# Performance work log

Hardware: AMD Instinct MI355X
Metric: run time of the kernel (lower is better)

Reference implementation:

```python
import jax, jax.numpy as jnp
import numpy as np

N_NODES = 50000
N_EDGES = 800000
D_FEAT = 64
N_AGENTS = 1024
A_DIM = 16
MSG = 128          # msg_dim
OUT = 128          # out_dim


def _w(k, fan_in, fan_out):
    return jax.random.normal(k, (fan_in, fan_out), jnp.float32) / np.sqrt(fan_in).astype(np.float32)


def setup_inputs() -> dict:
    key = jax.random.key(0)
    ks = jax.random.split(key, 24)
    inp = {}
    inp["x"] = jax.random.normal(ks[0], (N_NODES, D_FEAT), jnp.float32)
    inp["actions"] = jax.random.normal(ks[1], (N_AGENTS, A_DIM), jnp.float32)
    inp["senders"] = jax.random.randint(ks[2], (N_EDGES,), 0, N_NODES, jnp.int32)
    inp["receivers"] = jax.random.randint(ks[3], (N_EDGES,), 0, N_NODES, jnp.int32)
    inp["n_agents"] = N_AGENTS
    # message MLP: concat(sender, receiver) -> 256 -> 256 -> msg_dim
    inp["W_m1"] = _w(ks[4], 2 * D_FEAT, 256); inp["b_m1"] = jnp.zeros((256,), jnp.float32)
    inp["W_m2"] = _w(ks[5], 256, 256);        inp["b_m2"] = jnp.zeros((256,), jnp.float32)
    inp["W_m3"] = _w(ks[6], 256, MSG);        inp["b_m3"] = jnp.zeros((MSG,), jnp.float32)
    # aggregation MLP: msg_dim -> 128 -> 128 -> msg_dim
    inp["W_a1"] = _w(ks[7], MSG, 128);        inp["b_a1"] = jnp.zeros((128,), jnp.float32)
    inp["W_a2"] = _w(ks[8], 128, 128);        inp["b_a2"] = jnp.zeros((128,), jnp.float32)
    inp["W_a3"] = _w(ks[9], 128, MSG);        inp["b_a3"] = jnp.zeros((MSG,), jnp.float32)
    # update MLP: concat(node, aggregated) -> 256 -> 256 -> out_dim
    inp["W_u1"] = _w(ks[10], D_FEAT + MSG, 256); inp["b_u1"] = jnp.zeros((256,), jnp.float32)
    inp["W_u2"] = _w(ks[11], 256, 256);          inp["b_u2"] = jnp.zeros((256,), jnp.float32)
    inp["W_u3"] = _w(ks[12], 256, OUT);          inp["b_u3"] = jnp.zeros((OUT,), jnp.float32)
    # critic head
    inp["W_act"] = _w(ks[13], A_DIM, 128);    inp["b_act"] = jnp.zeros((128,), jnp.float32)
    inp["W_h1"] = _w(ks[14], OUT + 128, 256); inp["b_h1"] = jnp.zeros((256,), jnp.float32)
    inp["W_h2"] = _w(ks[15], 256, 256);       inp["b_h2"] = jnp.zeros((256,), jnp.float32)
    inp["W_q"] = _w(ks[16], 256, 1);          inp["b_q"] = jnp.zeros((1,), jnp.float32)
    return inp


def reference(x, actions, senders, receivers, n_agents,
              W_m1, b_m1, W_m2, b_m2, W_m3, b_m3,
              W_a1, b_a1, W_a2, b_a2, W_a3, b_a3,
              W_u1, b_u1, W_u2, b_u2, W_u3, b_u3,
              W_act, b_act, W_h1, b_h1, W_h2, b_h2, W_q, b_q):
    relu = jax.nn.relu
    # --- GNN layer: edge messages (gather endpoints, MLP) ---
    h = jnp.concatenate([x[senders], x[receivers]], axis=-1)   # [E, 2*D]
    h = relu(h @ W_m1 + b_m1)
    h = relu(h @ W_m2 + b_m2)
    msg = h @ W_m3 + b_m3                                      # [E, MSG]
    # --- aggregate messages at receivers (scatter-add) ---
    aggr = jax.ops.segment_sum(msg, receivers, num_segments=x.shape[0])  # [N, MSG]
    a = relu(aggr @ W_a1 + b_a1)
    a = relu(a @ W_a2 + b_a2)
    a = a @ W_a3 + b_a3                                        # [N, MSG]
    # --- node update ---
    u = jnp.concatenate([x, a], axis=-1)                       # [N, D+MSG]
    u = relu(u @ W_u1 + b_u1)
    u = relu(u @ W_u2 + b_u2)
    feats = (u @ W_u3 + b_u3)[:n_agents]                       # agent (type-0) nodes
    # --- critic head ---
    ap = relu(actions @ W_act + b_act)                         # [n_agents, 128]
    z = jnp.concatenate([feats, ap], axis=-1)
    z = relu(z @ W_h1 + b_h1)
    z = relu(z @ W_h2 + b_h2)
    q = z @ W_q + b_q
    return jnp.squeeze(q, axis=-1)                             # [n_agents]
```

## Files before the change

### kernel.cpp

```cpp
#include <hip/hip_runtime.h>
#include <hip/hip_bf16.h>


#define STRIDE 260

typedef __attribute__((ext_vector_type(8))) short short8;
typedef __attribute__((ext_vector_type(4))) float floatx4;

union Frag8 { short8 s; uint u[4]; };

__device__ __forceinline__ void cvt_hi_lo(const float4 f0, const float4 f1,
                                          Frag8& hi, Frag8& lo) {
    uint U[8] = { __float_as_uint(f0.x), __float_as_uint(f0.y),
                  __float_as_uint(f0.z), __float_as_uint(f0.w),
                  __float_as_uint(f1.x), __float_as_uint(f1.y),
                  __float_as_uint(f1.z), __float_as_uint(f1.w) };
    float F[8] = { f0.x, f0.y, f0.z, f0.w, f1.x, f1.y, f1.z, f1.w };
#pragma unroll
    for (int p = 0; p < 4; ++p) {
        uint a = U[2*p], b = U[2*p+1];
        hi.u[p] = (a >> 16) | (b & 0xFFFF0000u);
        float l0 = F[2*p]   - __uint_as_float(a & 0xFFFF0000u);
        float l1 = F[2*p+1] - __uint_as_float(b & 0xFFFF0000u);
        __hip_bfloat162 pl = __float22bfloat162_rn(make_float2(l0, l1));
        union { __hip_bfloat162 h; uint v; } cvt; cvt.h = pl;
        lo.u[p] = cvt.v;
    }
}

__global__ void pack_weights(const float* __restrict__ Wm1,
                             const float* __restrict__ Wm2,
                             const float* __restrict__ Wm3,
                             uint* __restrict__ pack) {
    int g = blockIdx.x * 256 + threadIdx.x;
    const float* W; int NOUT, NT, local; uint *dhi, *dlo;
    if (g < 4096)       { W = Wm1; NOUT = 256; NT = 16; local = g;         dhi = pack;          dlo = pack + 16384; }
    else if (g < 12288) { W = Wm2; NOUT = 256; NT = 16; local = g - 4096;  dhi = pack + 32768;  dlo = pack + 65536; }
    else                { W = Wm3; NOUT = 128; NT = 8;  local = g - 12288; dhi = pack + 98304;  dlo = pack + 114688; }
    int lane = local & 63;
    int tmp  = local >> 6;
    int nt = tmp % NT, kb = tmp / NT;
    int n  = nt * 16 + (lane & 15);
    int k0 = kb * 32 + ((lane >> 4) & 3) * 8;
    uint hi[4], lo[4];
#pragma unroll
    for (int p = 0; p < 4; ++p) {
        float f0 = W[(size_t)(k0 + 2*p)     * NOUT + n];
        float f1 = W[(size_t)(k0 + 2*p + 1) * NOUT + n];
        uint U0 = __float_as_uint(f0), U1 = __float_as_uint(f1);
        hi[p] = (U0 >> 16) | (U1 & 0xFFFF0000u);
        float l0 = f0 - __uint_as_float(U0 & 0xFFFF0000u);
        float l1 = f1 - __uint_as_float(U1 & 0xFFFF0000u);
        __hip_bfloat162 pl = __float22bfloat162_rn(make_float2(l0, l1));
        union { __hip_bfloat162 h; uint v; } cvt; cvt.h = pl;
        lo[p] = cvt.v;
    }
    int idx = ((kb * NT + nt) * 64 + lane) * 4;
    *(uint4*)(dhi + idx) = make_uint4(hi[0], hi[1], hi[2], hi[3]);
    *(uint4*)(dlo + idx) = make_uint4(lo[0], lo[1], lo[2], lo[3]);
}

#define FILT_CHUNK 4096
__global__ void filter_edges(const int* __restrict__ senders,
                             const int* __restrict__ receivers,
                             int E, int n_agents, int cap,
                             int* __restrict__ counter, int2* __restrict__ edges) {
    __shared__ int lcount;
    __shared__ int lbase;
    __shared__ int2 lbuf[FILT_CHUNK];
    const int t = (int)threadIdx.x;
    if (t == 0) lcount = 0;
    __syncthreads();
    int start = blockIdx.x * FILT_CHUNK;
    int end = min(start + FILT_CHUNK, E);
    for (int b0 = start; b0 < end; b0 += 256) {
        int idx = b0 + t;
        int r = -1, s = 0;
        bool pred = false;
        if (idx < end) {
            r = receivers[idx];
            pred = (r < n_agents);
            if (pred) s = senders[idx];
        }
        unsigned long long m = __ballot(pred);
        int lane = t & 63;
        int below = __popcll(m & ((1ull << lane) - 1));
        int cnt = __popcll(m);
        int wbase = 0;
        if (lane == 0 && cnt) wbase = atomicAdd(&lcount, cnt);
        wbase = __shfl(wbase, 0, 64);
        if (pred) lbuf[wbase + below] = make_int2(s, r);
    }
    __syncthreads();
    if (t == 0) lbase = atomicAdd(counter, lcount);
    __syncthreads();
    for (int i = t; i < lcount; i += 256) {
        int pos = lbase + i;
        if (pos < cap) edges[pos] = lbuf[i];
    }
}

template<int NIN, int NOUT, bool RELU>
__device__ __forceinline__ void mfma_layer(const float* in_lds, float* out_lds,
                                           const uint4* __restrict__ Whi,
                                           const uint4* __restrict__ Wlo,
                                           const float* __restrict__ b) {
    constexpr int KB  = NIN / 32;
    constexpr int NT  = NOUT / 16;
    constexpr int NTW = NT / 4;
    const int t    = (int)threadIdx.x;
    const int wave = t >> 6;
    const int l15  = t & 15;
    const int quad = (t >> 4) & 3;

    floatx4 acc[2][NTW];
#pragma unroll
    for (int mt = 0; mt < 2; ++mt)
#pragma unroll
        for (int i = 0; i < NTW; ++i) acc[mt][i] = (floatx4){0.f, 0.f, 0.f, 0.f};

#pragma unroll 2
    for (int kb = 0; kb < KB; ++kb) {
        Frag8 ahi[2], alo[2];
#pragma unroll
        for (int mt = 0; mt < 2; ++mt) {
            const float* src = in_lds + (mt * 16 + l15) * STRIDE + kb * 32 + quad * 8;
            float4 f0 = *(const float4*)src;
            float4 f1 = *(const float4*)(src + 4);
            cvt_hi_lo(f0, f1, ahi[mt], alo[mt]);
        }
#pragma unroll
        for (int i = 0; i < NTW; ++i) {
            int nt = wave * NTW + i;
            int widx = (kb * NT + nt) * 64 + (t & 63);
            Frag8 bhi, blo;
            *(uint4*)bhi.u = Whi[widx];
            *(uint4*)blo.u = Wlo[widx];
#pragma unroll
            for (int mt = 0; mt < 2; ++mt) {
                acc[mt][i] = __builtin_amdgcn_mfma_f32_16x16x32_bf16(alo[mt].s, bhi.s, acc[mt][i], 0, 0, 0);
                acc[mt][i] = __builtin_amdgcn_mfma_f32_16x16x32_bf16(ahi[mt].s, blo.s, acc[mt][i], 0, 0, 0);
                acc[mt][i] = __builtin_amdgcn_mfma_f32_16x16x32_bf16(ahi[mt].s, bhi.s, acc[mt][i], 0, 0, 0);
            }
        }
    }
#pragma unroll
    for (int i = 0; i < NTW; ++i) {
        int n = (wave * NTW + i) * 16 + l15;
        float bias = b[n];
#pragma unroll
        for (int mt = 0; mt < 2; ++mt) {
#pragma unroll
            for (int r = 0; r < 4; ++r) {
                float v = acc[mt][i][r] + bias;
                if (RELU) v = fmaxf(v, 0.f);
                out_lds[(mt * 16 + quad * 4 + r) * STRIDE + n] = v;
            }
        }
    }
}

#define ETE 32
__global__ __launch_bounds__(256, 2)
void edge_mlp(const float* __restrict__ x, const int2* __restrict__ edges,
              const int* __restrict__ counter, int cap, float* __restrict__ aggr,
              const uint* __restrict__ pack,
              const float* __restrict__ bm1, const float* __restrict__ bm2,
              const float* __restrict__ bm3) {
    __shared__ float bufA[ETE * STRIDE];
    __shared__ float bufB[ETE * STRIDE];
    __shared__ int sL[ETE], rL[ETE];
    const uint4* W1hi = (const uint4*)(pack);
    const uint4* W1lo = (const uint4*)(pack + 16384);
    const uint4* W2hi = (const uint4*)(pack + 32768);
    const uint4* W2lo = (const uint4*)(pack + 65536);
    const uint4* W3hi = (const uint4*)(pack + 98304);
    const uint4* W3lo = (const uint4*)(pack + 114688);
    const int count = min(counter[0], cap);
    const int ntiles = (count + ETE - 1) / ETE;
    const int t = (int)threadIdx.x;
    for (int tile = (int)blockIdx.x; tile < ntiles; tile += (int)gridDim.x) {
        const int base = tile * ETE;
        if (t < ETE) {
            int eg = base + t;
            int2 ed = (eg < count) ? edges[eg] : make_int2(0, -1);
            sL[t] = ed.x; rL[t] = ed.y;
        }
        __syncthreads();
        for (int idx = t; idx < ETE * 32; idx += 256) {
            int e = idx >> 5;
            int f4 = (idx & 31) * 4;
            int node = (f4 < 64) ? sL[e] : rL[e];
            float4 v = make_float4(0.f, 0.f, 0.f, 0.f);
            if (rL[e] >= 0) v = *(const float4*)(x + (size_t)node * 64 + (f4 & 63));
            *(float4*)(bufA + e * STRIDE + f4) = v;
        }
        __syncthreads();
        mfma_layer<128, 256, true >(bufA, bufB, W1hi, W1lo, bm1);
        __syncthreads();
        mfma_layer<256, 256, true >(bufB, bufA, W2hi, W2lo, bm2);
        __syncthreads();
        mfma_layer<256, 128, false>(bufA, bufB, W3hi, W3lo, bm3);
        __syncthreads();
        for (int idx = t; idx < ETE * 128; idx += 256) {
            int e = idx >> 7, o = idx & 127;
            if (base + e < count) {
                atomicAdd(&aggr[(size_t)rL[e] * 128 + o], bufB[e * STRIDE + o]);
            }
        }
        __syncthreads();
    }
}

template<int TE, int NIN, int NOUT, int COLS, int KS, bool RELU, int OOFF, int UNR>
__device__ __forceinline__ void mlp_layer(const float* in_lds, float* out_lds,
                                          float* part_lds,
                                          const float* __restrict__ W,
                                          const float* __restrict__ b) {
    constexpr int TX = NOUT / COLS;
    constexpr int NG = 256 / TX;
    static_assert(NG % KS == 0, "k-splits divide groups");
    constexpr int RG = NG / KS;
    static_assert(TE % RG == 0, "rows divide row-groups");
    constexpr int ER = TE / RG;
    constexpr int KRANGE = NIN / KS;
    static_assert(KRANGE % 4 == 0, "k-range multiple of 4");

    const int t   = (int)threadIdx.x;
    const int tx  = t % TX;
    const int grp = t / TX;
    const int ks  = grp % KS;
    const int rg  = grp / KS;
    const int o   = tx * COLS;
    const int e0  = rg * ER;
    const int k0  = ks * KRANGE;

    float acc[ER][COLS];
#pragma unroll
    for (int er = 0; er < ER; ++er)
#pragma unroll
        for (int c = 0; c < COLS; ++c) acc[er][c] = 0.f;

#pragma unroll UNR
    for (int kb = 0; kb < KRANGE; kb += 4) {
        const int k = k0 + kb;
        float w[4][COLS];
#pragma unroll
        for (int j = 0; j < 4; ++j) {
            const float* wp = W + (size_t)(k + j) * NOUT + o;
            if (COLS == 4) {
                float4 v = *(const float4*)wp;
                w[j][0] = v.x; w[j][1] = v.y; w[j][2] = v.z; w[j][3] = v.w;
            } else {
                float2 v = *(const float2*)wp;
                w[j][0] = v.x; w[j][1] = v.y;
            }
        }
#pragma unroll
        for (int er = 0; er < ER; ++er) {
            float4 a = *(const float4*)(in_lds + (e0 + er) * STRIDE + k);
#pragma unroll
            for (int c = 0; c < COLS; ++c) {
                acc[er][c] += a.x * w[0][c] + a.y * w[1][c]
                            + a.z * w[2][c] + a.w * w[3][c];
            }
        }
    }

    if (KS == 1) {
#pragma unroll
        for (int er = 0; er < ER; ++er) {
            float v[COLS];
#pragma unroll
            for (int c = 0; c < COLS; ++c) {
                v[c] = acc[er][c] + b[o + c];
                if (RELU) v[c] = fmaxf(v[c], 0.f);
            }
            float* dst = out_lds + (e0 + er) * STRIDE + OOFF + o;
            if (COLS == 4) *(float4*)dst = make_float4(v[0], v[1], v[2], v[3]);
            else           *(float2*)dst = make_float2(v[0], v[1]);
        }
    } else {
        if (ks != 0) {
            float* pr = (ks == 1) ? out_lds : part_lds + (size_t)(ks - 2) * TE * STRIDE;
#pragma unroll
            for (int er = 0; er < ER; ++er) {
                float* dst = pr + (e0 + er) * STRIDE + OOFF + o;
                if (COLS == 4) *(float4*)dst = make_float4(acc[er][0], acc[er][1],
                                                           acc[er][2], acc[er][3]);
                else           *(float2*)dst = make_float2(acc[er][0], acc[er][1]);
            }
        }
        __syncthreads();
        if (ks == 0) {
#pragma unroll
            for (int er = 0; er < ER; ++er) {
                float v[COLS];
#pragma unroll
                for (int c = 0; c < COLS; ++c) v[c] = acc[er][c];
#pragma unroll
                for (int j = 1; j < KS; ++j) {
                    const float* pr = (j == 1) ? out_lds
                                               : part_lds + (size_t)(j - 2) * TE * STRIDE;
                    const float* src = pr + (e0 + er) * STRIDE + OOFF + o;
                    if (COLS == 4) {
                        float4 p = *(const float4*)src;
                        v[0] += p.x; v[1] += p.y; v[2] += p.z; v[3] += p.w;
                    } else {
                        float2 p = *(const float2*)src;
                        v[0] += p.x; v[1] += p.y;
                    }
                }
#pragma unroll
                for (int c = 0; c < COLS; ++c) {
                    v[c] += b[o + c];
                    if (RELU) v[c] = fmaxf(v[c], 0.f);
                }
                float* dst = out_lds + (e0 + er) * STRIDE + OOFF + o;
                if (COLS == 4) *(float4*)dst = make_float4(v[0], v[1], v[2], v[3]);
                else           *(float2*)dst = make_float2(v[0], v[1]);
            }
        }
    }
}

#define NTE 4
__global__ __launch_bounds__(256, 1)
void node_update(const float* __restrict__ x, const float* __restrict__ actions,
                 const float* __restrict__ aggr, int n_agents,
                 const float* __restrict__ Wa1, const float* __restrict__ ba1,
                 const float* __restrict__ Wa2, const float* __restrict__ ba2,
                 const float* __restrict__ Wa3, const float* __restrict__ ba3,
                 const float* __restrict__ Wu1, const float* __restrict__ bu1,
                 const float* __restrict__ Wu2, const float* __restrict__ bu2,
                 const float* __restrict__ Wu3, const float* __restrict__ bu3,
                 const float* __restrict__ Wact, const float* __restrict__ bact,
                 const float* __restrict__ Wh1, const float* __restrict__ bh1,
                 const float* __restrict__ Wh2, const float* __restrict__ bh2,
                 const float* __restrict__ Wq,  const float* __restrict__ bq,
                 float* __restrict__ out) {
    __shared__ float bufA[NTE * STRIDE];
    __shared__ float bufB[NTE * STRIDE];
    __shared__ float bufP[2 * NTE * STRIDE];
    const int t = (int)threadIdx.x;
    const int base = (int)blockIdx.x * NTE;

    if (t < NTE * 32) {
        int e = t >> 5, f4 = (t & 31) * 4;
        int node = base + e;
        float4 v = make_float4(0.f, 0.f, 0.f, 0.f);
        if (node < n_agents) v = *(const float4*)(aggr + (size_t)node * 128 + f4);
        *(float4*)(bufA + e * STRIDE + f4) = v;
    }
    __syncthreads();
    mlp_layer<NTE, 128, 128, 2, 4, true,  0, 8>(bufA, bufB, bufP, Wa1, ba1); __syncthreads();
    mlp_layer<NTE, 128, 128, 2, 4, true,  0, 8>(bufB, bufA, bufP, Wa2, ba2); __syncthreads();
    mlp_layer<NTE, 128, 128, 2, 4, false, 0, 8>(bufA, bufB, bufP, Wa3, ba3); __syncthreads();
    if (t < NTE * 16) {
        int e = t >> 4, f4 = (t & 15) * 4;
        int node = base + e;
        float4 v = make_float4(0.f, 0.f, 0.f, 0.f);
        if (node < n_agents) v = *(const float4*)(x + (size_t)node * 64 + f4);
        *(float4*)(bufA + e * STRIDE + f4) = v;
    }
    if (t < NTE * 32) {
        int e = t >> 5, f4 = (t & 31) * 4;
        *(float4*)(bufA + e * STRIDE + 64 + f4) = *(const float4*)(bufB + e * STRIDE + f4);
    }
    __syncthreads();
    mlp_layer<NTE, 192, 256, 4, 4, true,  0, 4>(bufA, bufB, bufP, Wu1, bu1); __syncthreads();
    mlp_layer<NTE, 256, 256, 4, 4, true,  0, 4>(bufB, bufA, bufP, Wu2, bu2); __syncthreads();
    mlp_layer<NTE, 256, 128, 2, 4, false, 0, 4>(bufA, bufB, bufP, Wu3, bu3); __syncthreads();
    if (t < NTE * 4) {
        int e = t >> 2, f4 = (t & 3) * 4;
        int node = base + e;
        float4 v = make_float4(0.f, 0.f, 0.f, 0.f);
        if (node < n_agents) v = *(const float4*)(actions + (size_t)node * 16 + f4);
        *(float4*)(bufA + e * STRIDE + f4) = v;
    }
    __syncthreads();
    mlp_layer<NTE, 16,  128, 2, 4, true, 128, 1>(bufA, bufB, bufP, Wact, bact); __syncthreads();
    mlp_layer<NTE, 256, 256, 4, 4, true, 0,   4>(bufB, bufA, bufP, Wh1, bh1); __syncthreads();
    mlp_layer<NTE, 256, 256, 4, 4, true, 0,   4>(bufA, bufB, bufP, Wh2, bh2); __syncthreads();
    {
        int wv = t >> 6, lane = t & 63;
        int node = base + wv;
        float4 z = *(const float4*)(bufB + wv * STRIDE + lane * 4);
        float4 qw = *(const float4*)(Wq + lane * 4);
        float p = z.x * qw.x + z.y * qw.y + z.z * qw.z + z.w * qw.w;
#pragma unroll
        for (int off = 32; off >= 1; off >>= 1) p += __shfl_down(p, off, 64);
        if (lane == 0 && node < n_agents) out[node] = p + bq[0];
    }
}

extern "C" void kernel_launch(void* const* d_in, const int* in_sizes, int n_in,
                              void* d_out, int out_size, void* d_ws, size_t ws_size,
                              hipStream_t stream) {
    const float* x        = (const float*)d_in[0];
    const float* actions  = (const float*)d_in[1];
    const int*   senders  = (const int*)d_in[2];
    const int*   receivers= (const int*)d_in[3];
    const float* Wm1 = (const float*)d_in[5],  *bm1 = (const float*)d_in[6];
    const float* Wm2 = (const float*)d_in[7],  *bm2 = (const float*)d_in[8];
    const float* Wm3 = (const float*)d_in[9],  *bm3 = (const float*)d_in[10];
    const float* Wa1 = (const float*)d_in[11], *ba1 = (const float*)d_in[12];
    const float* Wa2 = (const float*)d_in[13], *ba2 = (const float*)d_in[14];
    const float* Wa3 = (const float*)d_in[15], *ba3 = (const float*)d_in[16];
    const float* Wu1 = (const float*)d_in[17], *bu1 = (const float*)d_in[18];
    const float* Wu2 = (const float*)d_in[19], *bu2 = (const float*)d_in[20];
    const float* Wu3 = (const float*)d_in[21], *bu3 = (const float*)d_in[22];
    const float* Wact= (const float*)d_in[23], *bact= (const float*)d_in[24];
    const float* Wh1 = (const float*)d_in[25], *bh1 = (const float*)d_in[26];
    const float* Wh2 = (const float*)d_in[27], *bh2 = (const float*)d_in[28];
    const float* Wq  = (const float*)d_in[29], *bq  = (const float*)d_in[30];

    const int E = in_sizes[2];
    const int n_agents = out_size;

    char* ws = (char*)d_ws;
    int*   counter = (int*)ws;
    float* aggr    = (float*)(ws + 1024);
    const size_t packOff = 1024 + (size_t)n_agents * 128 * sizeof(float);
    uint*  pack    = (uint*)(ws + packOff);
    const size_t edgeOff = packOff + 524288;
    int2*  edges   = (int2*)(ws + edgeOff);
    int cap = (int)((ws_size > edgeOff) ? (ws_size - edgeOff) / sizeof(int2) : 0);
    if (cap > E) cap = E;

    hipMemsetAsync(ws, 0, packOff, stream);

    pack_weights<<<64, 256, 0, stream>>>(Wm1, Wm2, Wm3, pack);

    int fblocks = (E + FILT_CHUNK - 1) / FILT_CHUNK;
    filter_edges<<<fblocks, 256, 0, stream>>>(senders, receivers, E, n_agents,
                                              cap, counter, edges);

    edge_mlp<<<512, 256, 0, stream>>>(x, edges, counter, cap, aggr, pack,
                                      bm1, bm2, bm3);

    node_update<<<(n_agents + NTE - 1) / NTE, 256, 0, stream>>>(
        x, actions, aggr, n_agents,
        Wa1, ba1, Wa2, ba2, Wa3, ba3,
        Wu1, bu1, Wu2, bu2, Wu3, bu3,
        Wact, bact, Wh1, bh1, Wh2, bh2, Wq, bq,
        (float*)d_out);
}
```

Before: 198.5 us.

## Run node-update and critic MLPs on split-bf16 MFMA and fuse pack with filter

Moves the node-side MLPs (aggregation, update, critic head) from scalar fp32 FMA loops onto 16-row split-bf16 MFMA tiles, using weights pre-packed into hi/lo bf16 fragments. Weight packing for all eleven matrices is merged into the edge-filter kernel's launch, removing one kernel launch. Node blocks grow from 4 to 16 agents, and the action projection and final q reduction are rewritten as small scalar loops. Weights are now packed with round-to-nearest for the hi part; precision stays near fp32 via three MFMAs per product, but the 64-block node grid may underuse the GPU.

```diff
diff --git a/kernel.cpp b/kernel.cpp
--- a/kernel.cpp
+++ b/kernel.cpp
@@ -6,7 +6,6 @@
 
 typedef __attribute__((ext_vector_type(8))) short short8;
 typedef __attribute__((ext_vector_type(4))) float floatx4;
-
 union Frag8 { short8 s; uint u[4]; };
 
 __device__ __forceinline__ void cvt_hi_lo(const float4 f0, const float4 f1,
@@ -28,76 +27,94 @@
     }
 }
 
-__global__ void pack_weights(const float* __restrict__ Wm1,
-                             const float* __restrict__ Wm2,
-                             const float* __restrict__ Wm3,
-                             uint* __restrict__ pack) {
-    int g = blockIdx.x * 256 + threadIdx.x;
-    const float* W; int NOUT, NT, local; uint *dhi, *dlo;
-    if (g < 4096)       { W = Wm1; NOUT = 256; NT = 16; local = g;         dhi = pack;          dlo = pack + 16384; }
-    else if (g < 12288) { W = Wm2; NOUT = 256; NT = 16; local = g - 4096;  dhi = pack + 32768;  dlo = pack + 65536; }
-    else                { W = Wm3; NOUT = 128; NT = 8;  local = g - 12288; dhi = pack + 98304;  dlo = pack + 114688; }
+__device__ __forceinline__ uint f2bf(float f) {
+    uint u = __float_as_uint(f);
+    return (u + 0x7FFFu + ((u >> 16) & 1u)) >> 16;
+}
+__device__ __forceinline__ float bf2f(uint h) { return __uint_as_float(h << 16); }
+__device__ __forceinline__ uint split2(float f0, float f1, uint& lo) {
+    uint h0 = f2bf(f0), h1 = f2bf(f1);
+    uint l0 = f2bf(f0 - bf2f(h0)), l1 = f2bf(f1 - bf2f(h1));
+    lo = l0 | (l1 << 16);
+    return h0 | (h1 << 16);
+}
+
+constexpr int PK_NIN[11]  = {128,256,256, 128,128,128, 192,256,256, 256,256};
+constexpr int PK_NOUT[11] = {256,256,128, 128,128,128, 256,256,128, 256,256};
+constexpr int pk_entries(int m) { return (PK_NIN[m]/32)*(PK_NOUT[m]/16)*64; }
+constexpr int pk_cum(int m) { int s = 0; for (int i = 0; i < m; ++i) s += pk_entries(i); return s; }
+constexpr int PK_TOTAL = pk_cum(11);
+constexpr int pk_off_hi(int m) { return 2*pk_cum(m); }
+constexpr int pk_off_lo(int m) { return 2*pk_cum(m) + pk_entries(m); }
+
+struct PackPtrs { const float* W[11]; };
+
+#define FILT_CHUNK 4096
+
+__global__ void pack_and_filter(PackPtrs P, uint4* __restrict__ pack,
+                                const int* __restrict__ senders,
+                                const int* __restrict__ receivers,
+                                int E, int n_agents, int cap,
+                                int* __restrict__ counter,
+                                int2* __restrict__ edges, int FB) {
+    __shared__ int lcount;
+    __shared__ int lbase;
+    __shared__ int2 lbuf[FILT_CHUNK];
+    const int t = (int)threadIdx.x;
+    if ((int)blockIdx.x < FB) {
+        if (t == 0) lcount = 0;
+        __syncthreads();
+        int start = blockIdx.x * FILT_CHUNK;
+        int end = min(start + FILT_CHUNK, E);
+        for (int b0 = start; b0 < end; b0 += 256) {
+            int idx = b0 + t;
+            int r = -1, s = 0;
+            bool pred = false;
+            if (idx < end) {
+                r = receivers[idx];
+                pred = (r < n_agents);
+                if (pred) s = senders[idx];
+            }
+            unsigned long long m = __ballot(pred);
+            int lane = t & 63;
+            int below = __popcll(m & ((1ull << lane) - 1));
+            int cnt = __popcll(m);
+            int wbase = 0;
+            if (lane == 0 && cnt) wbase = atomicAdd(&lcount, cnt);
+            wbase = __shfl(wbase, 0, 64);
+            if (pred) lbuf[wbase + below] = make_int2(s, r);
+        }
+        __syncthreads();
+        if (t == 0) lbase = atomicAdd(counter, lcount);
+        __syncthreads();
+        for (int i = t; i < lcount; i += 256) {
+            int pos = lbase + i;
+            if (pos < cap) edges[pos] = lbuf[i];
+        }
+        return;
+    }
+    int g = ((int)blockIdx.x - FB) * 256 + t;
+    if (g >= PK_TOTAL) return;
+    int m = 0;
+#pragma unroll
+    for (int i = 1; i < 11; ++i) if (g >= pk_cum(i)) m = i;
+    int local = g - pk_cum(m);
+    const float* W = P.W[m];
+    int NOUT = PK_NOUT[m], NT = NOUT / 16;
     int lane = local & 63;
     int tmp  = local >> 6;
     int nt = tmp % NT, kb = tmp / NT;
     int n  = nt * 16 + (lane & 15);
-    int k0 = kb * 32 + ((lane >> 4) & 3) * 8;
+    int k0 = kb * 32 + (lane >> 4) * 8;
     uint hi[4], lo[4];
 #pragma unroll
     for (int p = 0; p < 4; ++p) {
         float f0 = W[(size_t)(k0 + 2*p)     * NOUT + n];
         float f1 = W[(size_t)(k0 + 2*p + 1) * NOUT + n];
-        uint U0 = __float_as_uint(f0), U1 = __float_as_uint(f1);
-        hi[p] = (U0 >> 16) | (U1 & 0xFFFF0000u);
-        float l0 = f0 - __uint_as_float(U0 & 0xFFFF0000u);
-        float l1 = f1 - __uint_as_float(U1 & 0xFFFF0000u);
-        __hip_bfloat162 pl = __float22bfloat162_rn(make_float2(l0, l1));
-        union { __hip_bfloat162 h; uint v; } cvt; cvt.h = pl;
-        lo[p] = cvt.v;
-    }
-    int idx = ((kb * NT + nt) * 64 + lane) * 4;
-    *(uint4*)(dhi + idx) = make_uint4(hi[0], hi[1], hi[2], hi[3]);
-    *(uint4*)(dlo + idx) = make_uint4(lo[0], lo[1], lo[2], lo[3]);
-}
-
-#define FILT_CHUNK 4096
-__global__ void filter_edges(const int* __restrict__ senders,
-                             const int* __restrict__ receivers,
-                             int E, int n_agents, int cap,
-                             int* __restrict__ counter, int2* __restrict__ edges) {
-    __shared__ int lcount;
-    __shared__ int lbase;
-    __shared__ int2 lbuf[FILT_CHUNK];
-    const int t = (int)threadIdx.x;
-    if (t == 0) lcount = 0;
-    __syncthreads();
-    int start = blockIdx.x * FILT_CHUNK;
-    int end = min(start + FILT_CHUNK, E);
-    for (int b0 = start; b0 < end; b0 += 256) {
-        int idx = b0 + t;
-        int r = -1, s = 0;
-        bool pred = false;
-        if (idx < end) {
-            r = receivers[idx];
-            pred = (r < n_agents);
-            if (pred) s = senders[idx];
-        }
-        unsigned long long m = __ballot(pred);
-        int lane = t & 63;
-        int below = __popcll(m & ((1ull << lane) - 1));
-        int cnt = __popcll(m);
-        int wbase = 0;
-        if (lane == 0 && cnt) wbase = atomicAdd(&lcount, cnt);
-        wbase = __shfl(wbase, 0, 64);
-        if (pred) lbuf[wbase + below] = make_int2(s, r);
-    }
-    __syncthreads();
-    if (t == 0) lbase = atomicAdd(counter, lcount);
-    __syncthreads();
-    for (int i = t; i < lcount; i += 256) {
-        int pos = lbase + i;
-        if (pos < cap) edges[pos] = lbuf[i];
-    }
+        hi[p] = split2(f0, f1, lo[p]);
+    }
+    pack[pk_off_hi(m) + local] = make_uint4(hi[0], hi[1], hi[2], hi[3]);
+    pack[pk_off_lo(m) + local] = make_uint4(lo[0], lo[1], lo[2], lo[3]);
 }
 
 template<int NIN, int NOUT, bool RELU>
@@ -160,22 +177,70 @@
     }
 }
 
+template<int NIN, int NOUT, bool RELU, int OOFF>
+__device__ __forceinline__ void mfma_layer16(const float* in_lds, float* out_lds,
+                                             const uint4* __restrict__ Whi,
+                                             const uint4* __restrict__ Wlo,
+                                             const float* __restrict__ b) {
+    constexpr int KB  = NIN / 32;
+    constexpr int NT  = NOUT / 16;
+    constexpr int NTW = NT / 4;
+    const int t    = (int)threadIdx.x;
+    const int wave = t >> 6;
+    const int l15  = t & 15;
+    const int quad = (t >> 4) & 3;
+
+    floatx4 acc[NTW];
+#pragma unroll
+    for (int i = 0; i < NTW; ++i) acc[i] = (floatx4){0.f, 0.f, 0.f, 0.f};
+
+#pragma unroll 2
+    for (int kb = 0; kb < KB; ++kb) {
+        Frag8 ahi, alo;
+        const float* src = in_lds + l15 * STRIDE + kb * 32 + quad * 8;
+        float4 f0 = *(const float4*)src;
+        float4 f1 = *(const float4*)(src + 4);
+        cvt_hi_lo(f0, f1, ahi, alo);
+#pragma unroll
+        for (int i = 0; i < NTW; ++i) {
+            int widx = (kb * NT + wave * NTW + i) * 64 + (t & 63);
+            Frag8 bhi, blo;
+            *(uint4*)bhi.u = Whi[widx];
+            *(uint4*)blo.u = Wlo[widx];
+            acc[i] = __builtin_amdgcn_mfma_f32_16x16x32_bf16(alo.s, bhi.s, acc[i], 0, 0, 0);
+            acc[i] = __builtin_amdgcn_mfma_f32_16x16x32_bf16(ahi.s, blo.s, acc[i], 0, 0, 0);
+            acc[i] = __builtin_amdgcn_mfma_f32_16x16x32_bf16(ahi.s, bhi.s, acc[i], 0, 0, 0);
+        }
+    }
+#pragma unroll
+    for (int i = 0; i < NTW; ++i) {
+        int n = (wave * NTW + i) * 16 + l15;
+        float bias = b[n];
+#pragma unroll
+        for (int r = 0; r < 4; ++r) {
+            float v = acc[i][r] + bias;
+            if (RELU) v = fmaxf(v, 0.f);
+            out_lds[(quad * 4 + r) * STRIDE + OOFF + n] = v;
+        }
+    }
+}
+
 #define ETE 32
 __global__ __launch_bounds__(256, 2)
 void edge_mlp(const float* __restrict__ x, const int2* __restrict__ edges,
               const int* __restrict__ counter, int cap, float* __restrict__ aggr,
-              const uint* __restrict__ pack,
+              const uint4* __restrict__ pack,
               const float* __restrict__ bm1, const float* __restrict__ bm2,
               const float* __restrict__ bm3) {
     __shared__ float bufA[ETE * STRIDE];
     __shared__ float bufB[ETE * STRIDE];
     __shared__ int sL[ETE], rL[ETE];
-    const uint4* W1hi = (const uint4*)(pack);
-    const uint4* W1lo = (const uint4*)(pack + 16384);
-    const uint4* W2hi = (const uint4*)(pack + 32768);
-    const uint4* W2lo = (const uint4*)(pack + 65536);
-    const uint4* W3hi = (const uint4*)(pack + 98304);
-    const uint4* W3lo = (const uint4*)(pack + 114688);
+    const uint4* W1hi = pack + pk_off_hi(0);
+    const uint4* W1lo = pack + pk_off_lo(0);
+    const uint4* W2hi = pack + pk_off_hi(1);
+    const uint4* W2lo = pack + pk_off_lo(1);
+    const uint4* W3hi = pack + pk_off_hi(2);
+    const uint4* W3lo = pack + pk_off_lo(2);
     const int count = min(counter[0], cap);
     const int ntiles = (count + ETE - 1) / ETE;
     const int t = (int)threadIdx.x;
@@ -212,185 +277,90 @@
     }
 }
 
-template<int TE, int NIN, int NOUT, int COLS, int KS, bool RELU, int OOFF, int UNR>
-__device__ __forceinline__ void mlp_layer(const float* in_lds, float* out_lds,
-                                          float* part_lds,
-                                          const float* __restrict__ W,
-                                          const float* __restrict__ b) {
-    constexpr int TX = NOUT / COLS;
-    constexpr int NG = 256 / TX;
-    static_assert(NG % KS == 0, "k-splits divide groups");
-    constexpr int RG = NG / KS;
-    static_assert(TE % RG == 0, "rows divide row-groups");
-    constexpr int ER = TE / RG;
-    constexpr int KRANGE = NIN / KS;
-    static_assert(KRANGE % 4 == 0, "k-range multiple of 4");
-
-    const int t   = (int)threadIdx.x;
-    const int tx  = t % TX;
-    const int grp = t / TX;
-    const int ks  = grp % KS;
-    const int rg  = grp / KS;
-    const int o   = tx * COLS;
-    const int e0  = rg * ER;
-    const int k0  = ks * KRANGE;
-
-    float acc[ER][COLS];
-#pragma unroll
-    for (int er = 0; er < ER; ++er)
-#pragma unroll
-        for (int c = 0; c < COLS; ++c) acc[er][c] = 0.f;
-
-#pragma unroll UNR
-    for (int kb = 0; kb < KRANGE; kb += 4) {
-        const int k = k0 + kb;
-        float w[4][COLS];
-#pragma unroll
-        for (int j = 0; j < 4; ++j) {
-            const float* wp = W + (size_t)(k + j) * NOUT + o;
-            if (COLS == 4) {
-                float4 v = *(const float4*)wp;
-                w[j][0] = v.x; w[j][1] = v.y; w[j][2] = v.z; w[j][3] = v.w;
-            } else {
-                float2 v = *(const float2*)wp;
-                w[j][0] = v.x; w[j][1] = v.y;
-            }
-        }
-#pragma unroll
-        for (int er = 0; er < ER; ++er) {
-            float4 a = *(const float4*)(in_lds + (e0 + er) * STRIDE + k);
-#pragma unroll
-            for (int c = 0; c < COLS; ++c) {
-                acc[er][c] += a.x * w[0][c] + a.y * w[1][c]
-                            + a.z * w[2][c] + a.w * w[3][c];
-            }
-        }
-    }
-
-    if (KS == 1) {
-#pragma unroll
-        for (int er = 0; er < ER; ++er) {
-            float v[COLS];
-#pragma unroll
-            for (int c = 0; c < COLS; ++c) {
-                v[c] = acc[er][c] + b[o + c];
-                if (RELU) v[c] = fmaxf(v[c], 0.f);
-            }
-            float* dst = out_lds + (e0 + er) * STRIDE + OOFF + o;
-            if (COLS == 4) *(float4*)dst = make_float4(v[0], v[1], v[2], v[3]);
-            else           *(float2*)dst = make_float2(v[0], v[1]);
-        }
-    } else {
-        if (ks != 0) {
-            float* pr = (ks == 1) ? out_lds : part_lds + (size_t)(ks - 2) * TE * STRIDE;
-#pragma unroll
-            for (int er = 0; er < ER; ++er) {
-                float* dst = pr + (e0 + er) * STRIDE + OOFF + o;
-                if (COLS == 4) *(float4*)dst = make_float4(acc[er][0], acc[er][1],
-                                                           acc[er][2], acc[er][3]);
-                else           *(float2*)dst = make_float2(acc[er][0], acc[er][1]);
-            }
-        }
-        __syncthreads();
-        if (ks == 0) {
-#pragma unroll
-            for (int er = 0; er < ER; ++er) {
-                float v[COLS];
-#pragma unroll
-                for (int c = 0; c < COLS; ++c) v[c] = acc[er][c];
-#pragma unroll
-                for (int j = 1; j < KS; ++j) {
-                    const float* pr = (j == 1) ? out_lds
-                                               : part_lds + (size_t)(j - 2) * TE * STRIDE;
-                    const float* src = pr + (e0 + er) * STRIDE + OOFF + o;
-                    if (COLS == 4) {
-                        float4 p = *(const float4*)src;
-                        v[0] += p.x; v[1] += p.y; v[2] += p.z; v[3] += p.w;
-                    } else {
-                        float2 p = *(const float2*)src;
-                        v[0] += p.x; v[1] += p.y;
-                    }
-                }
-#pragma unroll
-                for (int c = 0; c < COLS; ++c) {
-                    v[c] += b[o + c];
-                    if (RELU) v[c] = fmaxf(v[c], 0.f);
-                }
-                float* dst = out_lds + (e0 + er) * STRIDE + OOFF + o;
-                if (COLS == 4) *(float4*)dst = make_float4(v[0], v[1], v[2], v[3]);
-                else           *(float2*)dst = make_float2(v[0], v[1]);
-            }
-        }
-    }
-}
-
-#define NTE 4
 __global__ __launch_bounds__(256, 1)
 void node_update(const float* __restrict__ x, const float* __restrict__ actions,
                  const float* __restrict__ aggr, int n_agents,
-                 const float* __restrict__ Wa1, const float* __restrict__ ba1,
-                 const float* __restrict__ Wa2, const float* __restrict__ ba2,
-                 const float* __restrict__ Wa3, const float* __restrict__ ba3,
-                 const float* __restrict__ Wu1, const float* __restrict__ bu1,
-                 const float* __restrict__ Wu2, const float* __restrict__ bu2,
-                 const float* __restrict__ Wu3, const float* __restrict__ bu3,
+                 const uint4* __restrict__ pack,
+                 const float* __restrict__ ba1, const float* __restrict__ ba2,
+                 const float* __restrict__ ba3,
+                 const float* __restrict__ bu1, const float* __restrict__ bu2,
+                 const float* __restrict__ bu3,
                  const float* __restrict__ Wact, const float* __restrict__ bact,
-                 const float* __restrict__ Wh1, const float* __restrict__ bh1,
-                 const float* __restrict__ Wh2, const float* __restrict__ bh2,
+                 const float* __restrict__ bh1, const float* __restrict__ bh2,
                  const float* __restrict__ Wq,  const float* __restrict__ bq,
                  float* __restrict__ out) {
-    __shared__ float bufA[NTE * STRIDE];
-    __shared__ float bufB[NTE * STRIDE];
-    __shared__ float bufP[2 * NTE * STRIDE];
+    __shared__ float bufA[16 * STRIDE];
+    __shared__ float bufB[16 * STRIDE];
+    __shared__ float qpart[16][17];
     const int t = (int)threadIdx.x;
-    const int base = (int)blockIdx.x * NTE;
-
-    if (t < NTE * 32) {
-        int e = t >> 5, f4 = (t & 31) * 4;
-        int node = base + e;
+    const int base = (int)blockIdx.x * 16;
+
+    for (int idx = t; idx < 16 * 32; idx += 256) {
+        int e = idx >> 5, f4 = (idx & 31) * 4;
         float4 v = make_float4(0.f, 0.f, 0.f, 0.f);
-        if (node < n_agents) v = *(const float4*)(aggr + (size_t)node * 128 + f4);
+        if (base + e < n_agents) v = *(const float4*)(aggr + (size_t)(base + e) * 128 + f4);
         *(float4*)(bufA + e * STRIDE + f4) = v;
     }
     __syncthreads();
-    mlp_layer<NTE, 128, 128, 2, 4, true,  0, 8>(bufA, bufB, bufP, Wa1, ba1); __syncthreads();
-    mlp_layer<NTE, 128, 128, 2, 4, true,  0, 8>(bufB, bufA, bufP, Wa2, ba2); __syncthreads();
-    mlp_layer<NTE, 128, 128, 2, 4, false, 0, 8>(bufA, bufB, bufP, Wa3, ba3); __syncthreads();
-    if (t < NTE * 16) {
-        int e = t >> 4, f4 = (t & 15) * 4;
-        int node = base + e;
+    mfma_layer16<128, 128, true,  0 >(bufA, bufB, pack + pk_off_hi(3), pack + pk_off_lo(3), ba1);
+    __syncthreads();
+    mfma_layer16<128, 128, true,  0 >(bufB, bufA, pack + pk_off_hi(4), pack + pk_off_lo(4), ba2);
+    __syncthreads();
+    mfma_layer16<128, 128, false, 64>(bufA, bufB, pack + pk_off_hi(5), pack + pk_off_lo(5), ba3);
+    for (int idx = t; idx < 16 * 16; idx += 256) {
+        int e = idx >> 4, f4 = (idx & 15) * 4;
         float4 v = make_float4(0.f, 0.f, 0.f, 0.f);
-        if (node < n_agents) v = *(const float4*)(x + (size_t)node * 64 + f4);
-        *(float4*)(bufA + e * STRIDE + f4) = v;
-    }
-    if (t < NTE * 32) {
-        int e = t >> 5, f4 = (t & 31) * 4;
-        *(float4*)(bufA + e * STRIDE + 64 + f4) = *(const float4*)(bufB + e * STRIDE + f4);
-    }
-    __syncthreads();
-    mlp_layer<NTE, 192, 256, 4, 4, true,  0, 4>(bufA, bufB, bufP, Wu1, bu1); __syncthreads();
-    mlp_layer<NTE, 256, 256, 4, 4, true,  0, 4>(bufB, bufA, bufP, Wu2, bu2); __syncthreads();
-    mlp_layer<NTE, 256, 128, 2, 4, false, 0, 4>(bufA, bufB, bufP, Wu3, bu3); __syncthreads();
-    if (t < NTE * 4) {
-        int e = t >> 2, f4 = (t & 3) * 4;
-        int node = base + e;
-        float4 v = make_float4(0.f, 0.f, 0.f, 0.f);
-        if (node < n_agents) v = *(const float4*)(actions + (size_t)node * 16 + f4);
-        *(float4*)(bufA + e * STRIDE + f4) = v;
-    }
-    __syncthreads();
-    mlp_layer<NTE, 16,  128, 2, 4, true, 128, 1>(bufA, bufB, bufP, Wact, bact); __syncthreads();
-    mlp_layer<NTE, 256, 256, 4, 4, true, 0,   4>(bufB, bufA, bufP, Wh1, bh1); __syncthreads();
-    mlp_layer<NTE, 256, 256, 4, 4, true, 0,   4>(bufA, bufB, bufP, Wh2, bh2); __syncthreads();
+        if (base + e < n_agents) v = *(const float4*)(x + (size_t)(base + e) * 64 + f4);
+        *(float4*)(bufB + e * STRIDE + f4) = v;
+    }
+    __syncthreads();
+    mfma_layer16<192, 256, true,  0 >(bufB, bufA, pack + pk_off_hi(6), pack + pk_off_lo(6), bu1);
+    __syncthreads();
+    mfma_layer16<256, 256, true,  0 >(bufA, bufB, pack + pk_off_hi(7), pack + pk_off_lo(7), bu2);
+    __syncthreads();
+    mfma_layer16<256, 128, false, 0 >(bufB, bufA, pack + pk_off_hi(8), pack + pk_off_lo(8), bu3);
     {
-        int wv = t >> 6, lane = t & 63;
-        int node = base + wv;
-        float4 z = *(const float4*)(bufB + wv * STRIDE + lane * 4);
-        float4 qw = *(const float4*)(Wq + lane * 4);
-        float p = z.x * qw.x + z.y * qw.y + z.z * qw.z + z.w * qw.w;
-#pragma unroll
-        for (int off = 32; off >= 1; off >>= 1) p += __shfl_down(p, off, 64);
-        if (lane == 0 && node < n_agents) out[node] = p + bq[0];
+        int e = t >> 4, c0 = (t & 15) * 8;
+        float accp[8];
+#pragma unroll
+        for (int c = 0; c < 8; ++c) accp[c] = bact[c0 + c];
+        if (base + e < n_agents) {
+#pragma unroll
+            for (int k = 0; k < 16; ++k) {
+                float av = actions[(size_t)(base + e) * 16 + k];
+#pragma unroll
+                for (int c = 0; c < 8; ++c)
+                    accp[c] += av * Wact[(size_t)k * 128 + c0 + c];
+            }
+        }
+#pragma unroll
+        for (int c = 0; c < 8; ++c)
+            bufA[e * STRIDE + 128 + c0 + c] = fmaxf(accp[c], 0.f);
+    }
+    __syncthreads();
+    mfma_layer16<256, 256, true, 0>(bufA, bufB, pack + pk_off_hi(9),  pack + pk_off_lo(9),  bh1);
+    __syncthreads();
+    mfma_layer16<256, 256, true, 0>(bufB, bufA, pack + pk_off_hi(10), pack + pk_off_lo(10), bh2);
+    __syncthreads();
+    {
+        int e = t >> 4, g = t & 15;
+        const float* z = bufA + e * STRIDE + g * 16;
+        const float* w = Wq + g * 16;
+        float p = 0.f;
+#pragma unroll
+        for (int j = 0; j < 16; j += 4) {
+            float4 zv = *(const float4*)(z + j);
+            float4 wv = *(const float4*)(w + j);
+            p += zv.x * wv.x + zv.y * wv.y + zv.z * wv.z + zv.w * wv.w;
+        }
+        qpart[e][g] = p;
+    }
+    __syncthreads();
+    if (t < 16 && base + t < n_agents) {
+        float s = bq[0];
+#pragma unroll
+        for (int g = 0; g < 16; ++g) s += qpart[t][g];
+        out[base + t] = s;
     }
 }
 
@@ -422,27 +392,31 @@
     int*   counter = (int*)ws;
     float* aggr    = (float*)(ws + 1024);
     const size_t packOff = 1024 + (size_t)n_agents * 128 * sizeof(float);
-    uint*  pack    = (uint*)(ws + packOff);
-    const size_t edgeOff = packOff + 524288;
+    uint4* pack    = (uint4*)(ws + packOff);
+    const size_t packBytes = (size_t)2 * PK_TOTAL * 16;
+    const size_t edgeOff = packOff + packBytes;
     int2*  edges   = (int2*)(ws + edgeOff);
     int cap = (int)((ws_size > edgeOff) ? (ws_size - edgeOff) / sizeof(int2) : 0);
     if (cap > E) cap = E;
 
     hipMemsetAsync(ws, 0, packOff, stream);
 
-    pack_weights<<<64, 256, 0, stream>>>(Wm1, Wm2, Wm3, pack);
-
-    int fblocks = (E + FILT_CHUNK - 1) / FILT_CHUNK;
-    filter_edges<<<fblocks, 256, 0, stream>>>(senders, receivers, E, n_agents,
-                                              cap, counter, edges);
+    PackPtrs P;
+    P.W[0] = Wm1; P.W[1] = Wm2; P.W[2] = Wm3;
+    P.W[3] = Wa1; P.W[4] = Wa2; P.W[5] = Wa3;
+    P.W[6] = Wu1; P.W[7] = Wu2; P.W[8] = Wu3;
+    P.W[9] = Wh1; P.W[10] = Wh2;
+    const int FB = (E + FILT_CHUNK - 1) / FILT_CHUNK;
+    const int PB = (PK_TOTAL + 255) / 256;
+    pack_and_filter<<<FB + PB, 256, 0, stream>>>(P, pack, senders, receivers,
+                                                 E, n_agents, cap, counter,
+                                                 edges, FB);
 
     edge_mlp<<<512, 256, 0, stream>>>(x, edges, counter, cap, aggr, pack,
                                       bm1, bm2, bm3);
 
-    node_update<<<(n_agents + NTE - 1) / NTE, 256, 0, stream>>>(
-        x, actions, aggr, n_agents,
-        Wa1, ba1, Wa2, ba2, Wa3, ba3,
-        Wu1, bu1, Wu2, bu2, Wu3, bu3,
-        Wact, bact, Wh1, bh1, Wh2, bh2, Wq, bq,
+    node_update<<<(n_agents + 15) / 16, 256, 0, stream>>>(
+        x, actions, aggr, n_agents, pack,
+        ba1, ba2, ba3, bu1, bu2, bu3, Wact, bact, bh1, bh2, Wq, bq,
         (float*)d_out);
 }
```

Result: no change. 195.5 us (-1.5%).
